# Optimization experiments

Measured on AMD Instinct MI355X. Metric: run time of the kernel, lower is better.

The kernel has to match this reference:

```python
import jax, jax.numpy as jnp
import numpy as np

B, N, D, K, H, DH, DEPTH, MULT = 1, 4096, 512, 256, 8, 64, 2, 4
EPS = 1e-5
SCALE = DH ** -0.5


def setup_inputs() -> dict:
    key = jax.random.key(0)
    ks = jax.random.split(key, 16)
    w = lambda k, shape, s: (jax.random.normal(k, shape, dtype=jnp.float32) * s)
    inp = {
        'x_real': jax.random.normal(ks[0], (B, N, D), dtype=jnp.float32),
        'x_imag': jax.random.normal(ks[1], (B, N, D), dtype=jnp.float32),
        # real-valued attention block params (shared by all 8 combos), stacked over depth
        'Wq': w(ks[2], (DEPTH, D, H * DH), 0.02), 'bq': jnp.zeros((DEPTH, H * DH), jnp.float32),
        'Wk': w(ks[3], (DEPTH, D, H * DH), 0.02), 'bk': jnp.zeros((DEPTH, H * DH), jnp.float32),
        'Wv': w(ks[4], (DEPTH, D, H * DH), 0.02), 'bv': jnp.zeros((DEPTH, H * DH), jnp.float32),
        'proj_k': w(ks[5], (DEPTH, N, K), 1.0 / np.sqrt(K)),
        'proj_v': w(ks[6], (DEPTH, N, K), 1.0 / np.sqrt(K)),
        'Wout': w(ks[7], (DEPTH, H * DH, D), 0.02), 'bout': jnp.zeros((DEPTH, D), jnp.float32),
        # complex FFN params
        'W1r': w(ks[8], (DEPTH, D, D * MULT), 0.02), 'W1i': w(ks[9], (DEPTH, D, D * MULT), 0.02),
        'b1r': jnp.zeros((DEPTH, D * MULT), jnp.float32), 'b1i': jnp.zeros((DEPTH, D * MULT), jnp.float32),
        'W2r': w(ks[10], (DEPTH, D * MULT, D), 0.02), 'W2i': w(ks[11], (DEPTH, D * MULT, D), 0.02),
        'b2r': jnp.zeros((DEPTH, D), jnp.float32), 'b2i': jnp.zeros((DEPTH, D), jnp.float32),
    }
    return inp


def _cln(xr, xi):
    # ComplexLayerNorm2d with elementwise_affine=False: complex whitening over last dim
    xr = xr - xr.mean(-1, keepdims=True)
    xi = xi - xi.mean(-1, keepdims=True)
    Crr = jnp.mean(xr * xr, -1) + EPS
    Cii = jnp.mean(xi * xi, -1) + EPS
    Cri = jnp.mean(xr * xi, -1)
    s = jnp.sqrt(Crr * Cii - Cri * Cri)
    t = jnp.sqrt(Cii + Crr + 2.0 * s)
    inv = 1.0 / (s * t)
    Rrr = ((Cii + s) * inv)[..., None]
    Rii = ((Crr + s) * inv)[..., None]
    Rri = (-Cri * inv)[..., None]
    return Rrr * xr + Rri * xi, Rii * xi + Rri * xr


def _attn_real(xq, xk, xv, Wq, bq, Wk, bk, Wv, bv, pk, pv, Wo, bo):
    # low-rank Linformer attention, NO softmax (attn = dots, as in source)
    Bc = xq.shape[0]
    q = (xq @ Wq + bq).reshape(Bc, N, H, DH).transpose(0, 2, 1, 3)           # bhnd
    keys = jnp.einsum('bnd,nk->bkd', xk @ Wk + bk, pk)                        # [Bc,K,H*DH]
    vals = jnp.einsum('bnd,nk->bkd', xv @ Wv + bv, pv)
    keys = keys.reshape(Bc, K, H, DH).transpose(0, 2, 1, 3)                   # bhkd
    vals = vals.reshape(Bc, K, H, DH).transpose(0, 2, 1, 3)
    dots = jnp.einsum('bhnd,bhkd->bhnk', q, keys) * SCALE
    out = jnp.einsum('bhnk,bhkd->bhnd', dots, vals)
    out = out.transpose(0, 2, 1, 3).reshape(Bc, N, H * DH)
    return out @ Wo + bo


def _complex_attn(xr, xi, p):
    A, Bm = xr, xi
    # combo order: (AAA),(AAB),(ABA),(BAA),(ABB),(BAB),(BBA),(BBB) stacked into batch
    Xq = jnp.concatenate([A, A, A, Bm, A, Bm, Bm, Bm], 0)
    Xk = jnp.concatenate([A, A, Bm, A, Bm, A, Bm, Bm], 0)
    Xv = jnp.concatenate([A, Bm, A, A, Bm, Bm, A, Bm], 0)
    o = _attn_real(Xq, Xk, Xv, *p).reshape(8, -1, N, D)
    out_r = o[0] - o[4] - o[5] - o[6]
    out_i = -o[7] + o[3] + o[2] + o[1]
    return out_r, out_i


def _ff(xr, xi, W1r, W1i, b1r, b1i, W2r, W2i, b2r, b2i):
    hr = xr @ W1r - xi @ W1i + b1r
    hi = xr @ W1i + xi @ W1r + b1i
    hr = jax.nn.relu(hr)  # GELU alias resolves to nn.ReLU in source
    hi = jax.nn.relu(hi)
    return hr @ W2r - hi @ W2i + b2r, hr @ W2i + hi @ W2r + b2i


def reference(x_real, x_imag, Wq, bq, Wk, bk, Wv, bv, proj_k, proj_v, Wout, bout,
              W1r, W1i, b1r, b1i, W2r, W2i, b2r, b2i):
    xr, xi = x_real, x_imag
    for d in range(DEPTH):
        nr, ni = _cln(xr, xi)
        ar, ai = _complex_attn(nr, ni, (Wq[d], bq[d], Wk[d], bk[d], Wv[d], bv[d],
                                        proj_k[d], proj_v[d], Wout[d], bout[d]))
        xr, xi = xr + ar, xi + ai
        nr, ni = _cln(xr, xi)
        fr, fi = _ff(nr, ni, W1r[d], W1i[d], b1r[d], b1i[d], W2r[d], W2i[d], b2r[d], b2i[d])
        xr, xi = xr + fr, xi + fi
    return jnp.stack([xr, xi])  # [2, B, N, D] real/imag
```

## Files before the change

### kernel.cpp

```cpp
#include <hip/hip_runtime.h>

#define NSEQ 4096
#define DM   512
#define KLR  256
#define HD   512
#define DFF  2048
#define SCALE 0.125f

typedef __attribute__((ext_vector_type(4))) float  f32x4;
typedef __attribute__((ext_vector_type(8))) short  short8;
typedef __attribute__((ext_vector_type(8))) __bf16 bf16x8;

__device__ __forceinline__ short f2bf(float f) {
  unsigned u = __float_as_uint(f);
  u = (u + 0x7fffu + ((u >> 16) & 1u)) >> 16;
  return (short)u;
}

__device__ __forceinline__ void gload_lds(const short* g, void* ldsbase) {
  __builtin_amdgcn_global_load_lds(
      (const __attribute__((address_space(1))) void*)g,
      (__attribute__((address_space(3))) void*)ldsbase, 16, 0, 0);
}

template<int BM, int BN, bool SK>
__global__ __launch_bounds__(256)
void gemm_f(const short* __restrict__ A, int lda, long sA,
            const short* __restrict__ B, int ldb, long sB,
            float* __restrict__ Cf, int ldc, long sCf,
            short* __restrict__ Cb, int ldcb, long sCb,
            short* __restrict__ Cb2, int negCb2,
            const float* __restrict__ bias, float bscale, int rowBias,
            int Kd, float alpha, float beta, int relu, int writeCf,
            int colSplit, long csOff)
{
  constexpr int WM = BM / 2, WN = BN / 2, FM = WM / 16, FN = WN / 16;
  constexpr int AISS = (BM * 64) / 4096, BISS = (BN * 64) / 4096;
  const int tid = threadIdx.x, bz = blockIdx.z;
  long kbeg = 0;
  if constexpr (SK) {
    const int half = bz & 1, kc = bz >> 1;
    A += (long)half * sA; B += (long)half * sB; Cf += (long)half * sCf;
    kbeg = (long)kc * Kd;
  } else {
    A += (long)bz * sA; B += (long)bz * sB;
    Cf += (long)bz * sCf; Cb += (long)bz * sCb;
  }
  const int bm0 = blockIdx.x * BM, bn0 = blockIdx.y * BN;
  __shared__ __align__(16) short As[BM * 32];
  __shared__ __align__(16) short Bs[BN * 32];
  const int wid = tid >> 6, lane = tid & 63;
  const int wr = wid >> 1, wc = wid & 1;
  const int lrow = lane & 15, lkc = lane >> 4;
  const int swz = (lkc ^ (lrow & 3)) << 3;

  f32x4 acc[FM][FN] = {};
  const int nK = Kd >> 5;
  for (int kt = 0; kt < nK; ++kt) {
    const long kg = kbeg + ((long)kt << 5);
    if (kt) __syncthreads();
    #pragma unroll
    for (int i = 0; i < AISS; ++i) {
      const int fb = i * 4096 + wid * 1024;
      const int f = fb + lane * 16;
      const int r = f >> 6, sl = (f >> 4) & 3;
      const int e = ((sl ^ (r & 3)) << 3);
      gload_lds(A + (long)(bm0 + r) * lda + kg + e, (char*)As + fb);
    }
    #pragma unroll
    for (int i = 0; i < BISS; ++i) {
      const int fb = i * 4096 + wid * 1024;
      const int f = fb + lane * 16;
      const int r = f >> 6, sl = (f >> 4) & 3;
      const int e = ((sl ^ (r & 3)) << 3);
      gload_lds(B + (long)(bn0 + r) * ldb + kg + e, (char*)Bs + fb);
    }
    __syncthreads();
    bf16x8 af[FM], bfv[FN];
    #pragma unroll
    for (int m = 0; m < FM; ++m)
      af[m] = *(const bf16x8*)(As + ((wr * WM + m * 16 + lrow) << 5) + swz);
    #pragma unroll
    for (int n = 0; n < FN; ++n)
      bfv[n] = *(const bf16x8*)(Bs + ((wc * WN + n * 16 + lrow) << 5) + swz);
    #pragma unroll
    for (int m = 0; m < FM; ++m)
      #pragma unroll
      for (int n = 0; n < FN; ++n)
        acc[m][n] = __builtin_amdgcn_mfma_f32_16x16x32_bf16(af[m], bfv[n], acc[m][n], 0, 0, 0);
  }

  #pragma unroll
  for (int m = 0; m < FM; ++m) {
    #pragma unroll
    for (int n = 0; n < FN; ++n) {
      const int row0 = bm0 + wr * WM + m * 16 + lkc * 4;
      const int col  = bn0 + wc * WN + n * 16 + lrow;
      float* cfp = Cf + ((col >= colSplit) ? csOff : 0);
      #pragma unroll
      for (int r = 0; r < 4; ++r) {
        if constexpr (SK) {
          atomicAdd(Cf + (long)(row0 + r) * ldc + col, alpha * acc[m][n][r]);
        } else {
          float v = alpha * acc[m][n][r];
          if (beta != 0.f) v += beta * cfp[(long)(row0 + r) * ldc + col];
          if (bias) v += bscale * bias[rowBias ? (row0 + r) : col];
          if (relu) v = fmaxf(v, 0.f);
          if (writeCf) cfp[(long)(row0 + r) * ldc + col] = v;
          if (Cb)  Cb [(long)(row0 + r) * ldcb + col] = f2bf(v);
          if (Cb2) Cb2[(long)(row0 + r) * ldcb + col] = f2bf(negCb2 ? -v : v);
        }
      }
    }
  }
}

__global__ __launch_bounds__(256)
void cln_k(const float* __restrict__ xr, const float* __restrict__ xi, short* __restrict__ ncat)
{
  const int row  = blockIdx.x * 4 + (threadIdx.x >> 6);
  const int lane = threadIdx.x & 63;
  const float* pr = xr + (long)row * DM + lane * 8;
  const float* pi = xi + (long)row * DM + lane * 8;
  f32x4 a0 = ((const f32x4*)pr)[0], a1 = ((const f32x4*)pr)[1];
  f32x4 b0 = ((const f32x4*)pi)[0], b1 = ((const f32x4*)pi)[1];
  float ar[8], ai[8];
  #pragma unroll
  for (int j = 0; j < 4; ++j) { ar[j] = a0[j]; ar[4 + j] = a1[j]; ai[j] = b0[j]; ai[4 + j] = b1[j]; }
  float sr = 0, si = 0, srr = 0, sii = 0, sri = 0;
  #pragma unroll
  for (int j = 0; j < 8; ++j) {
    sr += ar[j]; si += ai[j];
    srr += ar[j] * ar[j]; sii += ai[j] * ai[j]; sri += ar[j] * ai[j];
  }
  #pragma unroll
  for (int off = 32; off >= 1; off >>= 1) {
    sr  += __shfl_xor(sr, off);  si  += __shfl_xor(si, off);
    srr += __shfl_xor(srr, off); sii += __shfl_xor(sii, off); sri += __shfl_xor(sri, off);
  }
  const float inv512 = 1.f / 512.f;
  float mr = sr * inv512, mi = si * inv512;
  float Crr = srr * inv512 - mr * mr + 1e-5f;
  float Cii = sii * inv512 - mi * mi + 1e-5f;
  float Cri = sri * inv512 - mr * mi;
  float s = sqrtf(fmaxf(Crr * Cii - Cri * Cri, 0.f));
  float t = sqrtf(Crr + Cii + 2.f * s);
  float inv = 1.f / (s * t);
  float Rrr = (Cii + s) * inv, Rii = (Crr + s) * inv, Rri = -Cri * inv;
  short8 vr, vi;
  #pragma unroll
  for (int j = 0; j < 8; ++j) {
    float a = ar[j] - mr, b = ai[j] - mi;
    vr[j] = f2bf(Rrr * a + Rri * b);
    vi[j] = f2bf(Rii * b + Rri * a);
  }
  *(short8*)(ncat + (long)row * (2 * DM) + lane * 8) = vr;
  *(short8*)(ncat + (long)row * (2 * DM) + DM + lane * 8) = vi;
}

__global__ __launch_bounds__(256)
void e_k(const float* __restrict__ kvf, short* __restrict__ Eo)
{
  const int h = blockIdx.x;
  const int tid = threadIdx.x;
  const int wid = tid >> 6, lane = tid & 63;
  const int wr = wid >> 1, wc = wid & 1;
  const int lrow = lane & 15, lkc = lane >> 4;
  __shared__ short kaT[64 * 32], kbT2[64 * 32], vaT[64 * 32], vbT2[64 * 32];
  const float* kA = kvf + (long)h * 64;
  const float* kB = kA + (long)KLR * HD;
  const float* vA = kB + (long)KLR * HD;
  const float* vB = vA + (long)KLR * HD;
  f32x4 aAA[2][2] = {}, aBB[2][2] = {}, aAB[2][2] = {}, aBA[2][2] = {};
  const int kr = tid >> 3;
  const int dh0 = (tid & 7) * 8;
  for (int kt = 0; kt < 8; ++kt) {
    __syncthreads();
    const long krow = kt * 32 + kr;
    #pragma unroll
    for (int j = 0; j < 8; ++j) {
      const int dh = dh0 + j;
      kaT [dh * 32 + kr] = f2bf(kA[krow * HD + dh]);
      kbT2[dh * 32 + kr] = f2bf(kB[krow * HD + dh]);
      vaT [dh * 32 + kr] = f2bf(vA[krow * HD + dh]);
      vbT2[dh * 32 + kr] = f2bf(vB[krow * HD + dh]);
    }
    __syncthreads();
    bf16x8 fka[2], fkb[2], fva[2], fvb[2];
    #pragma unroll
    for (int m = 0; m < 2; ++m) {
      const int off = ((wr * 32 + m * 16 + lrow) << 5) + (lkc << 3);
      fka[m] = *(const bf16x8*)(kaT + off);
      fkb[m] = *(const bf16x8*)(kbT2 + off);
    }
    #pragma unroll
    for (int n = 0; n < 2; ++n) {
      const int off = ((wc * 32 + n * 16 + lrow) << 5) + (lkc << 3);
      fva[n] = *(const bf16x8*)(vaT + off);
      fvb[n] = *(const bf16x8*)(vbT2 + off);
    }
    #pragma unroll
    for (int m = 0; m < 2; ++m)
      #pragma unroll
      for (int n = 0; n < 2; ++n) {
        aAA[m][n] = __builtin_amdgcn_mfma_f32_16x16x32_bf16(fka[m], fva[n], aAA[m][n], 0, 0, 0);
        aBB[m][n] = __builtin_amdgcn_mfma_f32_16x16x32_bf16(fkb[m], fvb[n], aBB[m][n], 0, 0, 0);
        aAB[m][n] = __builtin_amdgcn_mfma_f32_16x16x32_bf16(fka[m], fvb[n], aAB[m][n], 0, 0, 0);
        aBA[m][n] = __builtin_amdgcn_mfma_f32_16x16x32_bf16(fkb[m], fva[n], aBA[m][n], 0, 0, 0);
      }
  }
  #pragma unroll
  for (int m = 0; m < 2; ++m)
    #pragma unroll
    for (int n = 0; n < 2; ++n) {
      const int row0 = wr * 32 + m * 16 + lkc * 4;
      const int col  = wc * 32 + n * 16 + lrow;
      #pragma unroll
      for (int r = 0; r < 4; ++r) {
        Eo[(long)h * 4096 + (row0 + r) * 64 + col]       = f2bf(SCALE * (aAA[m][n][r] - aBB[m][n][r]));
        Eo[(long)(8 + h) * 4096 + (row0 + r) * 64 + col] = f2bf(SCALE * (aAB[m][n][r] + aBA[m][n][r]));
      }
    }
}

__global__ __launch_bounds__(256)
void cvec_k(const float* __restrict__ FrT, const float* __restrict__ FiT,
            const float* __restrict__ bq, const float* __restrict__ bo, float* __restrict__ cv)
{
  const int j = blockIdx.x * 256 + threadIdx.x;
  float sr = 0.f, si = 0.f;
  for (int hd = 0; hd < HD; ++hd) {
    const float b = bq[hd];
    const float fr = FrT[(long)j * HD + hd], fi = FiT[(long)j * HD + hd];
    sr += b * (fr - fi); si += b * (fr + fi);
  }
  cv[j]       = sr - 2.f * bo[j];
  cv[512 + j] = si + 2.f * bo[j];
}

__global__ __launch_bounds__(256)
void tcvt2_k(const float* __restrict__ in, short* __restrict__ d1, float s1,
             short* __restrict__ d2, float s2, int R, int C, int ldo,
             long inZ, long outZ)
{
  __shared__ float tile[32][33];
  in += (long)blockIdx.z * inZ;
  d1 += (long)blockIdx.z * outZ;
  if (d2) d2 += (long)blockIdx.z * outZ;
  const int bx = blockIdx.x * 32, by = blockIdx.y * 32;
  const int x = threadIdx.x & 31, y = threadIdx.x >> 5;
  #pragma unroll
  for (int j = 0; j < 32; j += 8)
    tile[y + j][x] = in[(long)(by + y + j) * C + bx + x];
  __syncthreads();
  #pragma unroll
  for (int j = 0; j < 32; j += 8) {
    const float v = tile[x][y + j];
    const long o = (long)(bx + y + j) * ldo + by + x;
    d1[o] = f2bf(s1 * v);
    if (d2) d2[o] = f2bf(s2 * v);
  }
}

__global__ __launch_bounds__(256)
void cvt_k(const float* __restrict__ in, short* __restrict__ out, int n)
{
  const int i = (blockIdx.x * 256 + threadIdx.x) * 4;
  if (i >= n) return;
  f32x4 v = *(const f32x4*)(in + i);
  short tmp[4] = {f2bf(v[0]), f2bf(v[1]), f2bf(v[2]), f2bf(v[3])};
  *(unsigned long long*)(out + i) = *(unsigned long long*)tmp;
}

extern "C" void kernel_launch(void* const* d_in, const int* in_sizes, int n_in,
                              void* d_out, int out_size, void* d_ws, size_t ws_size,
                              hipStream_t stream)
{
  const float* x_real = (const float*)d_in[0];
  const float* x_imag = (const float*)d_in[1];
  const float* Wq  = (const float*)d_in[2];
  const float* bq  = (const float*)d_in[3];
  const float* Wk  = (const float*)d_in[4];
  const float* bk  = (const float*)d_in[5];
  const float* Wv  = (const float*)d_in[6];
  const float* bv  = (const float*)d_in[7];
  const float* pk  = (const float*)d_in[8];
  const float* pv  = (const float*)d_in[9];
  const float* Wo  = (const float*)d_in[10];
  const float* bo  = (const float*)d_in[11];
  const float* W1r = (const float*)d_in[12];
  const float* W1i = (const float*)d_in[13];
  const float* b1r = (const float*)d_in[14];
  const float* b1i = (const float*)d_in[15];
  const float* W2r = (const float*)d_in[16];
  const float* W2i = (const float*)d_in[17];
  const float* b2r = (const float*)d_in[18];
  const float* b2i = (const float*)d_in[19];

  float* xr = (float*)d_out;
  float* xi = xr + (long)NSEQ * DM;
  const int BIG = 1 << 30;
  const long XIOFF = (long)NSEQ * DM - 512;

  char* base = (char*)d_ws;
  size_t off = 0;
  auto alloc = [&](size_t bytes) -> char* {
    char* p = base + off; off += (bytes + 255) & ~(size_t)255; return p;
  };

  short* wkvT = (short*)alloc((size_t)2 * 1024 * 512 * 2);
  short* woT  = (short*)alloc((size_t)2 * DM * HD * 2);
  short* wqB  = (short*)alloc((size_t)2 * DM * HD * 2);
  short* w1c  = (short*)alloc((size_t)2 * 4096 * 1024 * 2);
  short* w2c  = (short*)alloc((size_t)2 * 1024 * 4096 * 2);
  short* pkT  = (short*)alloc((size_t)2 * KLR * NSEQ * 2);
  short* pvT  = (short*)alloc((size_t)2 * KLR * NSEQ * 2);
  float* bkvcat = (float*)alloc((size_t)2 * 1024 * 4);
  float* b1cat  = (float*)alloc((size_t)2 * 4096 * 4);
  float* b2cat  = (float*)alloc((size_t)2 * 1024 * 4);
  short* ncat  = (short*)alloc((size_t)NSEQ * 2 * DM * 2);
  short* kvbT  = (short*)alloc((size_t)1024 * 2 * NSEQ * 2);
  float* kvf   = (float*)alloc((size_t)4 * KLR * HD * 4);
  short* Eo    = (short*)alloc((size_t)16 * 64 * 64 * 2);
  float* FrT   = (float*)alloc((size_t)DM * HD * 4);
  float* FiT   = (float*)alloc((size_t)DM * HD * 4);
  short* FrTb  = (short*)alloc((size_t)DM * HD * 2);
  short* FiTb  = (short*)alloc((size_t)DM * HD * 2);
  short* BarBai= (short*)alloc((size_t)1024 * 1024 * 2);
  float* cv    = (float*)alloc((size_t)1024 * 4);
  short* hcat  = (short*)alloc((size_t)NSEQ * 2 * DFF * 2);
  if (off > ws_size) return;

  hipMemcpyAsync(xr, x_real, (size_t)NSEQ * DM * 4, hipMemcpyDeviceToDevice, stream);
  hipMemcpyAsync(xi, x_imag, (size_t)NSEQ * DM * 4, hipMemcpyDeviceToDevice, stream);

  tcvt2_k<<<dim3(HD/32, DM/32, 2), 256, 0, stream>>>(Wk, wkvT, 1.f, nullptr, 0.f, DM, HD, DM, (long)DM*HD, 524288);
  tcvt2_k<<<dim3(HD/32, DM/32, 2), 256, 0, stream>>>(Wv, wkvT + 512*512, 1.f, nullptr, 0.f, DM, HD, DM, (long)DM*HD, 524288);
  tcvt2_k<<<dim3(DM/32, HD/32, 2), 256, 0, stream>>>(Wo, woT, 1.f, nullptr, 0.f, HD, DM, HD, (long)HD*DM, 262144);
  cvt_k<<<2*DM*HD/1024, 256, 0, stream>>>(Wq, wqB, 2*DM*HD);
  tcvt2_k<<<dim3(DFF/32, DM/32, 2), 256, 0, stream>>>(W1r, w1c, 1.f, w1c + 2048*1024 + DM, 1.f, DM, DFF, 1024, (long)DM*DFF, 4194304);
  tcvt2_k<<<dim3(DFF/32, DM/32, 2), 256, 0, stream>>>(W1i, w1c + DM, -1.f, w1c + 2048*1024, 1.f, DM, DFF, 1024, (long)DM*DFF, 4194304);
  tcvt2_k<<<dim3(DM/32, DFF/32, 2), 256, 0, stream>>>(W2r, w2c, 1.f, w2c + 512*4096 + DFF, 1.f, DFF, DM, 4096, (long)DFF*DM, 4194304);
  tcvt2_k<<<dim3(DM/32, DFF/32, 2), 256, 0, stream>>>(W2i, w2c + DFF, -1.f, w2c + 512*4096, 1.f, DFF, DM, 4096, (long)DFF*DM, 4194304);
  tcvt2_k<<<dim3(KLR/32, NSEQ/32, 2), 256, 0, stream>>>(pk, pkT, 1.f, nullptr, 0.f, NSEQ, KLR, NSEQ, (long)NSEQ*KLR, 1048576);
  tcvt2_k<<<dim3(KLR/32, NSEQ/32, 2), 256, 0, stream>>>(pv, pvT, 1.f, nullptr, 0.f, NSEQ, KLR, NSEQ, (long)NSEQ*KLR, 1048576);
  for (int d = 0; d < 2; ++d) {
    hipMemcpyAsync(bkvcat + d*1024,       bk + d*HD,  HD*4,  hipMemcpyDeviceToDevice, stream);
    hipMemcpyAsync(bkvcat + d*1024 + 512, bv + d*HD,  HD*4,  hipMemcpyDeviceToDevice, stream);
    hipMemcpyAsync(b1cat + d*4096,        b1r + d*DFF, DFF*4, hipMemcpyDeviceToDevice, stream);
    hipMemcpyAsync(b1cat + d*4096 + 2048, b1i + d*DFF, DFF*4, hipMemcpyDeviceToDevice, stream);
    hipMemcpyAsync(b2cat + d*1024,        b2r + d*DM,  DM*4,  hipMemcpyDeviceToDevice, stream);
    hipMemcpyAsync(b2cat + d*1024 + 512,  b2i + d*DM,  DM*4,  hipMemcpyDeviceToDevice, stream);
  }

  for (int d = 0; d < 2; ++d) {
    const short* wkvT_d = wkvT + (long)d * 524288;
    const short* woT_d  = woT  + (long)d * 262144;
    const short* wqB_d  = wqB  + (long)d * 262144;
    const short* w1c_d  = w1c  + (long)d * 4194304;
    const short* w2c_d  = w2c  + (long)d * 4194304;
    const short* pkT_d  = pkT  + (long)d * 1048576;
    const short* pvT_d  = pvT  + (long)d * 1048576;
    const float* bq_d = bq + d * HD;   const float* bo_d = bo + d * DM;
    short* vbT = kvbT + (long)512 * 2 * NSEQ;

    cln_k<<<NSEQ/4, 256, 0, stream>>>(xr, xi, ncat);

    gemm_f<128,128,false><<<dim3(8, 32, 2), 256, 0, stream>>>(
      wkvT_d, 512, 0, ncat, 2*DM, DM, nullptr, 0, 0,
      kvbT, 2*NSEQ, NSEQ, nullptr, 0, bkvcat + d*1024, 1.f, 1, 512, 1.f, 0.f, 0, 0, BIG, 0);

    hipMemsetAsync(kvf, 0, (size_t)4 * KLR * HD * 4, stream);
    gemm_f<128,128,true><<<dim3(2, 4, 32), 256, 0, stream>>>(
      pkT_d, NSEQ, 0, kvbT, 2*NSEQ, NSEQ, kvf, HD, (long)KLR*HD, nullptr, 0, 0,
      nullptr, 0, nullptr, 0.f, 0, 256, 1.f, 0.f, 0, 0, BIG, 0);
    gemm_f<128,128,true><<<dim3(2, 4, 32), 256, 0, stream>>>(
      pvT_d, NSEQ, 0, vbT, 2*NSEQ, NSEQ, kvf + 2L*KLR*HD, HD, (long)KLR*HD, nullptr, 0, 0,
      nullptr, 0, nullptr, 0.f, 0, 256, 1.f, 0.f, 0, 0, BIG, 0);

    e_k<<<8, 256, 0, stream>>>(kvf, Eo);

    gemm_f<128,64,false><<<dim3(4, 1, 8), 256, 0, stream>>>(
      woT_d, HD, 64, Eo, 64, 4096, FrT, DM, 64, FrTb, DM, 64,
      nullptr, 0, nullptr, 0.f, 0, 64, 1.f, 0.f, 0, 1, BIG, 0);
    gemm_f<128,64,false><<<dim3(4, 1, 8), 256, 0, stream>>>(
      woT_d, HD, 64, Eo + 8L*4096, 64, 4096, FiT, DM, 64, FiTb, DM, 64,
      nullptr, 0, nullptr, 0.f, 0, 64, 1.f, 0.f, 0, 1, BIG, 0);

    gemm_f<128,128,false><<<dim3(4, 4, 1), 256, 0, stream>>>(
      FrTb, HD, 0, wqB_d, HD, 0, nullptr, 0, 0, BarBai, 2*DM, 0,
      BarBai + 512*1024 + DM, 0, nullptr, 0.f, 0, HD, 1.f, 0.f, 0, 0, BIG, 0);
    gemm_f<128,128,false><<<dim3(4, 4, 1), 256, 0, stream>>>(
      FiTb, HD, 0, wqB_d, HD, 0, nullptr, 0, 0, BarBai + 512*1024, 2*DM, 0,
      BarBai + DM, 1, nullptr, 0.f, 0, HD, 1.f, 0.f, 0, 0, BIG, 0);

    cvec_k<<<2, 256, 0, stream>>>(FrT, FiT, bq_d, bo_d, cv);

    gemm_f<64,128,false><<<dim3(64, 8, 1), 256, 0, stream>>>(
      ncat, 2*DM, 0, BarBai, 2*DM, 0, xr, DM, 0, nullptr, 0, 0,
      nullptr, 0, cv, 1.f, 0, 2*DM, 1.f, 1.f, 0, 1, 512, XIOFF);

    cln_k<<<NSEQ/4, 256, 0, stream>>>(xr, xi, ncat);

    gemm_f<128,128,false><<<dim3(32, 32, 1), 256, 0, stream>>>(
      ncat, 2*DM, 0, w1c_d, 2*DM, 0, nullptr, 0, 0, hcat, 2*DFF, 0,
      nullptr, 0, b1cat + d*4096, 1.f, 0, 2*DM, 1.f, 0.f, 1, 0, BIG, 0);

    gemm_f<64,128,false><<<dim3(64, 8, 1), 256, 0, stream>>>(
      hcat, 2*DFF, 0, w2c_d, 2*DFF, 0, xr, DM, 0, nullptr, 0, 0,
      nullptr, 0, b2cat + d*1024, 1.f, 0, 2*DFF, 1.f, 1.f, 0, 1, 512, XIOFF);
  }
}
```

Baseline: 909.9 us.

## Split-K residual GEMMs with atomics, batch Bar/Bai GEMMs, parallelize cvec, drop LDS swizzle

The residual-adding output-projection and FFN2 GEMMs become 2-way split-K launches with 128x128 tiles. Each K-slice atomically adds its partial result into xr/xi in place, and only the first slice adds the bias. The two Bar/Bai GEMMs merge into one batched launch with per-batch negation via a mask. cvec_k switches from one thread per output with a serial loop to one wavefront per output with vector loads and a shuffle reduction. The XOR swizzle on LDS tile loads and reads is removed, which simplifies addressing but may add LDS bank conflicts. Atomics also make the summation order nondeterministic.

```diff
diff --git a/kernel.cpp b/kernel.cpp
--- a/kernel.cpp
+++ b/kernel.cpp
@@ -29,22 +29,24 @@
             const short* __restrict__ B, int ldb, long sB,
             float* __restrict__ Cf, int ldc, long sCf,
             short* __restrict__ Cb, int ldcb, long sCb,
-            short* __restrict__ Cb2, int negCb2,
+            short* __restrict__ Cb2, long sCb2, int negMask,
             const float* __restrict__ bias, float bscale, int rowBias,
             int Kd, float alpha, float beta, int relu, int writeCf,
-            int colSplit, long csOff)
+            int colSplit, long csOff, int skH)
 {
   constexpr int WM = BM / 2, WN = BN / 2, FM = WM / 16, FN = WN / 16;
   constexpr int AISS = (BM * 64) / 4096, BISS = (BN * 64) / 4096;
   const int tid = threadIdx.x, bz = blockIdx.z;
   long kbeg = 0;
+  int kc = 0;
   if constexpr (SK) {
-    const int half = bz & 1, kc = bz >> 1;
+    const int half = bz % skH; kc = bz / skH;
     A += (long)half * sA; B += (long)half * sB; Cf += (long)half * sCf;
     kbeg = (long)kc * Kd;
   } else {
     A += (long)bz * sA; B += (long)bz * sB;
     Cf += (long)bz * sCf; Cb += (long)bz * sCb;
+    if (Cb2) Cb2 += (long)bz * sCb2;
   }
   const int bm0 = blockIdx.x * BM, bn0 = blockIdx.y * BN;
   __shared__ __align__(16) short As[BM * 32];
@@ -52,7 +54,6 @@
   const int wid = tid >> 6, lane = tid & 63;
   const int wr = wid >> 1, wc = wid & 1;
   const int lrow = lane & 15, lkc = lane >> 4;
-  const int swz = (lkc ^ (lrow & 3)) << 3;
 
   f32x4 acc[FM][FN] = {};
   const int nK = Kd >> 5;
@@ -63,26 +64,24 @@
     for (int i = 0; i < AISS; ++i) {
       const int fb = i * 4096 + wid * 1024;
       const int f = fb + lane * 16;
-      const int r = f >> 6, sl = (f >> 4) & 3;
-      const int e = ((sl ^ (r & 3)) << 3);
+      const int r = f >> 6, e = (f & 63) >> 1;
       gload_lds(A + (long)(bm0 + r) * lda + kg + e, (char*)As + fb);
     }
     #pragma unroll
     for (int i = 0; i < BISS; ++i) {
       const int fb = i * 4096 + wid * 1024;
       const int f = fb + lane * 16;
-      const int r = f >> 6, sl = (f >> 4) & 3;
-      const int e = ((sl ^ (r & 3)) << 3);
+      const int r = f >> 6, e = (f & 63) >> 1;
       gload_lds(B + (long)(bn0 + r) * ldb + kg + e, (char*)Bs + fb);
     }
     __syncthreads();
     bf16x8 af[FM], bfv[FN];
     #pragma unroll
     for (int m = 0; m < FM; ++m)
-      af[m] = *(const bf16x8*)(As + ((wr * WM + m * 16 + lrow) << 5) + swz);
+      af[m] = *(const bf16x8*)(As + ((wr * WM + m * 16 + lrow) << 5) + (lkc << 3));
     #pragma unroll
     for (int n = 0; n < FN; ++n)
-      bfv[n] = *(const bf16x8*)(Bs + ((wc * WN + n * 16 + lrow) << 5) + swz);
+      bfv[n] = *(const bf16x8*)(Bs + ((wc * WN + n * 16 + lrow) << 5) + (lkc << 3));
     #pragma unroll
     for (int m = 0; m < FM; ++m)
       #pragma unroll
@@ -100,7 +99,9 @@
       #pragma unroll
       for (int r = 0; r < 4; ++r) {
         if constexpr (SK) {
-          atomicAdd(Cf + (long)(row0 + r) * ldc + col, alpha * acc[m][n][r]);
+          float v = alpha * acc[m][n][r];
+          if (bias && kc == 0) v += bscale * bias[rowBias ? (row0 + r) : col];
+          atomicAdd(cfp + (long)(row0 + r) * ldc + col, v);
         } else {
           float v = alpha * acc[m][n][r];
           if (beta != 0.f) v += beta * cfp[(long)(row0 + r) * ldc + col];
@@ -108,7 +109,7 @@
           if (relu) v = fmaxf(v, 0.f);
           if (writeCf) cfp[(long)(row0 + r) * ldc + col] = v;
           if (Cb)  Cb [(long)(row0 + r) * ldcb + col] = f2bf(v);
-          if (Cb2) Cb2[(long)(row0 + r) * ldcb + col] = f2bf(negCb2 ? -v : v);
+          if (Cb2) Cb2[(long)(row0 + r) * ldcb + col] = f2bf(((negMask >> bz) & 1) ? -v : v);
         }
       }
     }
@@ -227,15 +228,28 @@
 void cvec_k(const float* __restrict__ FrT, const float* __restrict__ FiT,
             const float* __restrict__ bq, const float* __restrict__ bo, float* __restrict__ cv)
 {
-  const int j = blockIdx.x * 256 + threadIdx.x;
+  const int j = blockIdx.x * 4 + (threadIdx.x >> 6);
+  const int lane = threadIdx.x & 63;
+  const float* fr = FrT + (long)j * HD + lane * 8;
+  const float* fi = FiT + (long)j * HD + lane * 8;
+  const float* bp = bq + lane * 8;
+  f32x4 fr0 = ((const f32x4*)fr)[0], fr1 = ((const f32x4*)fr)[1];
+  f32x4 fi0 = ((const f32x4*)fi)[0], fi1 = ((const f32x4*)fi)[1];
+  f32x4 b0 = ((const f32x4*)bp)[0], b1 = ((const f32x4*)bp)[1];
   float sr = 0.f, si = 0.f;
-  for (int hd = 0; hd < HD; ++hd) {
-    const float b = bq[hd];
-    const float fr = FrT[(long)j * HD + hd], fi = FiT[(long)j * HD + hd];
-    sr += b * (fr - fi); si += b * (fr + fi);
-  }
-  cv[j]       = sr - 2.f * bo[j];
-  cv[512 + j] = si + 2.f * bo[j];
+  #pragma unroll
+  for (int t = 0; t < 4; ++t) {
+    sr += b0[t] * (fr0[t] - fi0[t]); si += b0[t] * (fr0[t] + fi0[t]);
+    sr += b1[t] * (fr1[t] - fi1[t]); si += b1[t] * (fr1[t] + fi1[t]);
+  }
+  #pragma unroll
+  for (int off = 32; off >= 1; off >>= 1) {
+    sr += __shfl_xor(sr, off); si += __shfl_xor(si, off);
+  }
+  if (lane == 0) {
+    cv[j]       = sr - 2.f * bo[j];
+    cv[512 + j] = si + 2.f * bo[j];
+  }
 }
 
 __global__ __launch_bounds__(256)
@@ -324,8 +338,7 @@
   short* Eo    = (short*)alloc((size_t)16 * 64 * 64 * 2);
   float* FrT   = (float*)alloc((size_t)DM * HD * 4);
   float* FiT   = (float*)alloc((size_t)DM * HD * 4);
-  short* FrTb  = (short*)alloc((size_t)DM * HD * 2);
-  short* FiTb  = (short*)alloc((size_t)DM * HD * 2);
+  short* FGb   = (short*)alloc((size_t)2 * DM * HD * 2);
   short* BarBai= (short*)alloc((size_t)1024 * 1024 * 2);
   float* cv    = (float*)alloc((size_t)1024 * 4);
   short* hcat  = (short*)alloc((size_t)NSEQ * 2 * DFF * 2);
@@ -368,46 +381,49 @@
 
     gemm_f<128,128,false><<<dim3(8, 32, 2), 256, 0, stream>>>(
       wkvT_d, 512, 0, ncat, 2*DM, DM, nullptr, 0, 0,
-      kvbT, 2*NSEQ, NSEQ, nullptr, 0, bkvcat + d*1024, 1.f, 1, 512, 1.f, 0.f, 0, 0, BIG, 0);
+      kvbT, 2*NSEQ, NSEQ, nullptr, 0, 0,
+      bkvcat + d*1024, 1.f, 1, 512, 1.f, 0.f, 0, 0, BIG, 0, 1);
 
     hipMemsetAsync(kvf, 0, (size_t)4 * KLR * HD * 4, stream);
     gemm_f<128,128,true><<<dim3(2, 4, 32), 256, 0, stream>>>(
-      pkT_d, NSEQ, 0, kvbT, 2*NSEQ, NSEQ, kvf, HD, (long)KLR*HD, nullptr, 0, 0,
-      nullptr, 0, nullptr, 0.f, 0, 256, 1.f, 0.f, 0, 0, BIG, 0);
+      pkT_d, NSEQ, 0, kvbT, 2*NSEQ, NSEQ, kvf, HD, (long)KLR*HD,
+      nullptr, 0, 0, nullptr, 0, 0,
+      nullptr, 0.f, 0, 256, 1.f, 0.f, 0, 0, BIG, 0, 2);
     gemm_f<128,128,true><<<dim3(2, 4, 32), 256, 0, stream>>>(
-      pvT_d, NSEQ, 0, vbT, 2*NSEQ, NSEQ, kvf + 2L*KLR*HD, HD, (long)KLR*HD, nullptr, 0, 0,
-      nullptr, 0, nullptr, 0.f, 0, 256, 1.f, 0.f, 0, 0, BIG, 0);
+      pvT_d, NSEQ, 0, vbT, 2*NSEQ, NSEQ, kvf + 2L*KLR*HD, HD, (long)KLR*HD,
+      nullptr, 0, 0, nullptr, 0, 0,
+      nullptr, 0.f, 0, 256, 1.f, 0.f, 0, 0, BIG, 0, 2);
 
     e_k<<<8, 256, 0, stream>>>(kvf, Eo);
 
     gemm_f<128,64,false><<<dim3(4, 1, 8), 256, 0, stream>>>(
-      woT_d, HD, 64, Eo, 64, 4096, FrT, DM, 64, FrTb, DM, 64,
-      nullptr, 0, nullptr, 0.f, 0, 64, 1.f, 0.f, 0, 1, BIG, 0);
+      woT_d, HD, 64, Eo, 64, 4096, FrT, DM, 64, FGb, DM, 64,
+      nullptr, 0, 0, nullptr, 0.f, 0, 64, 1.f, 0.f, 0, 1, BIG, 0, 1);
     gemm_f<128,64,false><<<dim3(4, 1, 8), 256, 0, stream>>>(
-      woT_d, HD, 64, Eo + 8L*4096, 64, 4096, FiT, DM, 64, FiTb, DM, 64,
-      nullptr, 0, nullptr, 0.f, 0, 64, 1.f, 0.f, 0, 1, BIG, 0);
-
-    gemm_f<128,128,false><<<dim3(4, 4, 1), 256, 0, stream>>>(
-      FrTb, HD, 0, wqB_d, HD, 0, nullptr, 0, 0, BarBai, 2*DM, 0,
-      BarBai + 512*1024 + DM, 0, nullptr, 0.f, 0, HD, 1.f, 0.f, 0, 0, BIG, 0);
-    gemm_f<128,128,false><<<dim3(4, 4, 1), 256, 0, stream>>>(
-      FiTb, HD, 0, wqB_d, HD, 0, nullptr, 0, 0, BarBai + 512*1024, 2*DM, 0,
-      BarBai + DM, 1, nullptr, 0.f, 0, HD, 1.f, 0.f, 0, 0, BIG, 0);
-
-    cvec_k<<<2, 256, 0, stream>>>(FrT, FiT, bq_d, bo_d, cv);
-
-    gemm_f<64,128,false><<<dim3(64, 8, 1), 256, 0, stream>>>(
-      ncat, 2*DM, 0, BarBai, 2*DM, 0, xr, DM, 0, nullptr, 0, 0,
-      nullptr, 0, cv, 1.f, 0, 2*DM, 1.f, 1.f, 0, 1, 512, XIOFF);
+      woT_d, HD, 64, Eo + 8L*4096, 64, 4096, FiT, DM, 64, FGb + 262144, DM, 64,
+      nullptr, 0, 0, nullptr, 0.f, 0, 64, 1.f, 0.f, 0, 1, BIG, 0, 1);
+
+    gemm_f<128,128,false><<<dim3(4, 4, 2), 256, 0, stream>>>(
+      FGb, HD, 262144, wqB_d, HD, 0, nullptr, 0, 0,
+      BarBai, 2*DM, 524288, BarBai + 524288 + DM, -524288L, 2,
+      nullptr, 0.f, 0, HD, 1.f, 0.f, 0, 0, BIG, 0, 1);
+
+    cvec_k<<<128, 256, 0, stream>>>(FrT, FiT, bq_d, bo_d, cv);
+
+    gemm_f<128,128,true><<<dim3(32, 8, 2), 256, 0, stream>>>(
+      ncat, 2*DM, 0, BarBai, 2*DM, 0, xr, DM, 0,
+      nullptr, 0, 0, nullptr, 0, 0,
+      cv, 1.f, 0, 512, 1.f, 0.f, 0, 0, 512, XIOFF, 1);
 
     cln_k<<<NSEQ/4, 256, 0, stream>>>(xr, xi, ncat);
 
     gemm_f<128,128,false><<<dim3(32, 32, 1), 256, 0, stream>>>(
       ncat, 2*DM, 0, w1c_d, 2*DM, 0, nullptr, 0, 0, hcat, 2*DFF, 0,
-      nullptr, 0, b1cat + d*4096, 1.f, 0, 2*DM, 1.f, 0.f, 1, 0, BIG, 0);
-
-    gemm_f<64,128,false><<<dim3(64, 8, 1), 256, 0, stream>>>(
-      hcat, 2*DFF, 0, w2c_d, 2*DFF, 0, xr, DM, 0, nullptr, 0, 0,
-      nullptr, 0, b2cat + d*1024, 1.f, 0, 2*DFF, 1.f, 1.f, 0, 1, 512, XIOFF);
-  }
-}
+      nullptr, 0, 0, b1cat + d*4096, 1.f, 0, 1024, 1.f, 0.f, 1, 0, BIG, 0, 1);
+
+    gemm_f<128,128,true><<<dim3(32, 8, 2), 256, 0, stream>>>(
+      hcat, 2*DFF, 0, w2c_d, 2*DFF, 0, xr, DM, 0,
+      nullptr, 0, 0, nullptr, 0, 0,
+      b2cat + d*1024, 1.f, 0, 2048, 1.f, 0.f, 0, 0, 512, XIOFF, 1);
+  }
+}
```

After: 852.5 us. 1.07x faster.
